# Kernel optimization log

Measured on AMD Instinct MI355X. Metric: run time of the kernel, lower is better.

The kernel has to match this reference:

```python
import jax, jax.numpy as jnp
import numpy as np

D_MODEL = 1024
NUM_HEADS = 16
HEAD_DIM = D_MODEL // NUM_HEADS
BATCH = 4
SEQ = 2048


def circulant(x, c, b):
    # Circulant linear layer via FFT: y = irfft(rfft(x) * rfft(c)) + b
    # x: (..., d), c: (d,), b: (d,)
    d = c.shape[0]
    y = jnp.fft.irfft(jnp.fft.rfft(x, axis=-1) * jnp.fft.rfft(c), n=d, axis=-1)
    return y + b


def setup_inputs() -> dict:
    key = jax.random.key(0)
    ks = jax.random.split(key, 9)
    scale = 1.0 / np.sqrt(D_MODEL)
    inp = {
        "x": jax.random.normal(ks[0], (BATCH, SEQ, D_MODEL), dtype=jnp.float32),
        "wq_c": jax.random.normal(ks[1], (D_MODEL,), dtype=jnp.float32) * scale,
        "wq_b": jnp.zeros((D_MODEL,), dtype=jnp.float32),
        "wk_c": jax.random.normal(ks[2], (D_MODEL,), dtype=jnp.float32) * scale,
        "wk_b": jnp.zeros((D_MODEL,), dtype=jnp.float32),
        "wv_c": jax.random.normal(ks[3], (D_MODEL,), dtype=jnp.float32) * scale,
        "wv_b": jnp.zeros((D_MODEL,), dtype=jnp.float32),
        "wo_c": jax.random.normal(ks[4], (D_MODEL,), dtype=jnp.float32) * scale,
        "wo_b": jnp.zeros((D_MODEL,), dtype=jnp.float32),
    }
    return inp


def reference(x, wq_c, wq_b, wk_c, wk_b, wv_c, wv_b, wo_c, wo_b):
    bs, seq_len, dm = x.shape
    Q = circulant(x, wq_c, wq_b)  # (B, S, D)
    K = circulant(x, wk_c, wk_b)
    V = circulant(x, wv_c, wv_b)
    Q = Q.reshape(bs, seq_len, NUM_HEADS, HEAD_DIM)
    K = K.reshape(bs, seq_len, NUM_HEADS, HEAD_DIM)
    V = V.reshape(bs, seq_len, NUM_HEADS, HEAD_DIM)
    scale = HEAD_DIM ** (-0.5)
    attn_logits = jnp.einsum("bqhd,bkhd->bhqk", Q, K) * scale  # (B, H, S, S)
    attn_weights = jax.nn.softmax(attn_logits, axis=-1)
    out_heads = jnp.einsum("bhqk,bkhd->bqhd", attn_weights, V)
    out_merge = out_heads.reshape(bs, seq_len, dm)
    out = circulant(out_merge, wo_c, wo_b)
    return out
```

## Files before the change

kernel.cpp:

```cpp
#include <hip/hip_runtime.h>
#include <hip/hip_bf16.h>

#define D_MODEL 1024
#define NUM_HEADS 16
#define HEAD_DIM 64
#define BATCH 4
#define SEQ 2048
#define MROWS (BATCH * SEQ)

using f32x4  = __attribute__((ext_vector_type(4))) float;
using bf16x8 = __attribute__((ext_vector_type(8))) short;

__device__ inline unsigned short f2bf(float f) {
    __hip_bfloat16 h = __float2bfloat16(f);
    return *reinterpret_cast<unsigned short*>(&h);
}

__device__ inline void gld_lds16(const unsigned short* g, unsigned short* l) {
    __builtin_amdgcn_global_load_lds(
        (const __attribute__((address_space(1))) unsigned int*)g,
        (__attribute__((address_space(3))) unsigned int*)l, 16, 0, 0);
}

#define QSCALE 0.18033688011112042f

__global__ __launch_bounds__(256) void prep(
    const float* __restrict__ cq, const float* __restrict__ ck,
    const float* __restrict__ cv, const float* __restrict__ co,
    const float* __restrict__ bq, const float* __restrict__ bk,
    const float* __restrict__ bv, const float* __restrict__ bo,
    unsigned short* __restrict__ Wt, float* __restrict__ bias,
    const float* __restrict__ x, unsigned short* __restrict__ xb)
{
    const int bid = blockIdx.x;
    const int t = threadIdx.x;
    if (bid < 4096) {
        const int n = bid;
        const int sel = n >> 10, nl = n & 1023;
        const float* c  = sel == 0 ? cq : sel == 1 ? ck : sel == 2 ? cv : co;
        const float* bb = sel == 0 ? bq : sel == 1 ? bk : sel == 2 ? bv : bo;
        const float sc = (sel == 0) ? QSCALE : 1.0f;
        ushort4 o;
        o.x = f2bf(sc * c[(nl - (4*t + 0)) & 1023]);
        o.y = f2bf(sc * c[(nl - (4*t + 1)) & 1023]);
        o.z = f2bf(sc * c[(nl - (4*t + 2)) & 1023]);
        o.w = f2bf(sc * c[(nl - (4*t + 3)) & 1023]);
        ((ushort4*)(Wt + (size_t)n * 1024))[t] = o;
        if (t == 0) bias[n] = sc * bb[nl];
    } else {
        const size_t i = (size_t)(bid - 4096) * 1024 + t * 4;
        float4 v = *(const float4*)(x + i);
        ushort4 o;
        o.x = f2bf(v.x); o.y = f2bf(v.y); o.z = f2bf(v.z); o.w = f2bf(v.w);
        *(ushort4*)(xb + i) = o;
    }
}

template <int OUT_MODE>
__global__ __launch_bounds__(256, 3) void gemm_circ(
    const unsigned short* __restrict__ A,
    const unsigned short* __restrict__ Bt,
    const float* __restrict__ bias,
    unsigned short* __restrict__ Qb, unsigned short* __restrict__ Kb,
    unsigned short* __restrict__ Vt, float* __restrict__ Cf)
{
    __shared__ unsigned short As[128 * 64];
    __shared__ unsigned short Bs[128 * 64];
    const int t = threadIdx.x;
    const int w = t >> 6, lane = t & 63;
    const int quad = lane >> 4, l16 = lane & 15;
    const int m0 = blockIdx.x * 128;
    const int n0 = blockIdx.y * 128;
    const int wm = (w & 1) * 64, wn = (w >> 1) * 64;

    f32x4 acc[4][4];
#pragma unroll
    for (int i = 0; i < 4; ++i)
#pragma unroll
        for (int j = 0; j < 4; ++j) acc[i][j] = (f32x4){0.f, 0.f, 0.f, 0.f};

    for (int k0 = 0; k0 < 1024; k0 += 64) {
        __syncthreads();
#pragma unroll
        for (int j = 0; j < 4; ++j) {
            const int s = j * 4 + w;
            const int i = s * 64 + lane;
            const int r = i >> 3;
            const int c = (i & 7) ^ (r & 7);
            gld_lds16(A  + (size_t)(m0 + r) * 1024 + k0 + c * 8, &As[s * 512]);
            gld_lds16(Bt + (size_t)(n0 + r) * 1024 + k0 + c * 8, &Bs[s * 512]);
        }
        __syncthreads();

#pragma unroll
        for (int kk = 0; kk < 2; ++kk) {
            bf16x8 af[4], bfr[4];
#pragma unroll
            for (int i = 0; i < 4; ++i) {
                const int r = wm + i * 16 + l16;
                const int slot = r * 8 + ((kk * 4 + quad) ^ (r & 7));
                af[i] = *(const bf16x8*)&As[slot * 8];
            }
#pragma unroll
            for (int j = 0; j < 4; ++j) {
                const int r = wn + j * 16 + l16;
                const int slot = r * 8 + ((kk * 4 + quad) ^ (r & 7));
                bfr[j] = *(const bf16x8*)&Bs[slot * 8];
            }
#pragma unroll
            for (int i = 0; i < 4; ++i)
#pragma unroll
                for (int j = 0; j < 4; ++j)
                    acc[i][j] = __builtin_amdgcn_mfma_f32_16x16x32_bf16(
                        af[i], bfr[j], acc[i][j], 0, 0, 0);
        }
    }

#pragma unroll
    for (int i = 0; i < 4; ++i) {
        const int gm = m0 + wm + i * 16 + quad * 4;
#pragma unroll
        for (int j = 0; j < 4; ++j) {
            const int gn = n0 + wn + j * 16 + l16;
            const float bv = bias[gn];
            if (OUT_MODE == 1) {
#pragma unroll
                for (int rr = 0; rr < 4; ++rr)
                    Cf[(size_t)(gm + rr) * 1024 + gn] = acc[i][j][rr] + bv;
            } else {
                const int sel = gn >> 10;
                if (sel == 0) {
#pragma unroll
                    for (int rr = 0; rr < 4; ++rr)
                        Qb[(size_t)(gm + rr) * 1024 + gn] = f2bf(acc[i][j][rr] + bv);
                } else if (sel == 1) {
                    const int col = gn & 1023;
#pragma unroll
                    for (int rr = 0; rr < 4; ++rr)
                        Kb[(size_t)(gm + rr) * 1024 + col] = f2bf(acc[i][j][rr] + bv);
                } else {
                    const int d = gn & 1023;
                    const int head = d >> 6, dl = d & 63;
                    const int b = gm >> 11, key = gm & 2047;
                    ushort4 vv;
                    vv.x = f2bf(acc[i][j][0] + bv);
                    vv.y = f2bf(acc[i][j][1] + bv);
                    vv.z = f2bf(acc[i][j][2] + bv);
                    vv.w = f2bf(acc[i][j][3] + bv);
                    *(ushort4*)&Vt[((size_t)((b * 16 + head) * 64 + dl)) * 2048 + key] = vv;
                }
            }
        }
    }
}

__global__ __launch_bounds__(256, 4) void attn_mfma(
    const unsigned short* __restrict__ Qb, const unsigned short* __restrict__ Kb,
    const unsigned short* __restrict__ Vt, unsigned short* __restrict__ O)
{
    __shared__ unsigned short Ks[2][64 * 64];
    __shared__ unsigned short Vs[2][64 * 64];

    const int t = threadIdx.x;
    const int w = t >> 6, lane = t & 63;
    const int quad = lane >> 4, l16 = lane & 15;
    const int bh = blockIdx.x;
    const int b = bh >> 4, head = bh & 15;
    const int qbase = blockIdx.y * 128 + w * 32;

    bf16x8 qa[2][2];
#pragma unroll
    for (int s = 0; s < 2; ++s)
#pragma unroll
        for (int h = 0; h < 2; ++h) {
            size_t off = (size_t)(b * SEQ + qbase + s*16 + l16) * D_MODEL
                       + head * HEAD_DIM + h*32 + quad*8;
            qa[s][h] = *(const bf16x8*)(Qb + off);
        }

    f32x4 acc[2][4];
    f32x4 acc_sum[2];
#pragma unroll
    for (int s = 0; s < 2; ++s) {
#pragma unroll
        for (int dt = 0; dt < 4; ++dt) acc[s][dt] = (f32x4){0.f,0.f,0.f,0.f};
        acc_sum[s] = (f32x4){0.f,0.f,0.f,0.f};
    }

    bf16x8 vones;
#pragma unroll
    for (int i = 0; i < 8; ++i) vones[i] = (short)0x3F80;

    const size_t kbase  = (size_t)(b * SEQ) * D_MODEL + head * HEAD_DIM;
    const size_t vtbase = (size_t)((b * NUM_HEADS + head) * HEAD_DIM) * SEQ;

#pragma unroll
    for (int j = 0; j < 2; ++j) {
        const int seg = j * 4 + w;
        const int i = seg * 64 + lane;
        const int r = i >> 3;
        const int ck = (i & 7) ^ ((r & 3) | ((r >> 1) & 4));
        const int cv = (i & 7) ^ (r & 7);
        gld_lds16(Kb + kbase + (size_t)r * D_MODEL + ck * 8, &Ks[0][seg * 512]);
        gld_lds16(Vt + vtbase + (size_t)r * SEQ + cv * 8, &Vs[0][seg * 512]);
    }

    int ib = 0;
    for (int kb = 0; kb < SEQ; kb += 64, ib ^= 1) {
        __syncthreads();

        if (kb + 64 < SEQ) {
#pragma unroll
            for (int j = 0; j < 2; ++j) {
                const int seg = j * 4 + w;
                const int i = seg * 64 + lane;
                const int r = i >> 3;
                const int ck = (i & 7) ^ ((r & 3) | ((r >> 1) & 4));
                const int cv = (i & 7) ^ (r & 7);
                gld_lds16(Kb + kbase + (size_t)(kb + 64 + r) * D_MODEL + ck * 8,
                          &Ks[ib ^ 1][seg * 512]);
                gld_lds16(Vt + vtbase + (size_t)r * SEQ + kb + 64 + cv * 8,
                          &Vs[ib ^ 1][seg * 512]);
            }
        }

        bf16x8 kf[2][2][2];
#pragma unroll
        for (int kh = 0; kh < 2; ++kh)
#pragma unroll
            for (int m = 0; m < 2; ++m) {
                const int r = kh * 32 + ((l16 >> 2) << 3) + m * 4 + (l16 & 3);
                const int sg = (r & 3) | ((r >> 1) & 4);
#pragma unroll
                for (int h = 0; h < 2; ++h) {
                    const int cc = (h * 4 + quad) ^ sg;
                    kf[kh][m][h] = *(const bf16x8*)&Ks[ib][(r * 8 + cc) * 8];
                }
            }

#pragma unroll
        for (int kh = 0; kh < 2; ++kh) {
            bf16x8 pf[2];
#pragma unroll
            for (int s = 0; s < 2; ++s) {
                f32x4 st0 = (f32x4){0.f,0.f,0.f,0.f};
                f32x4 st1 = (f32x4){0.f,0.f,0.f,0.f};
#pragma unroll
                for (int h = 0; h < 2; ++h) {
                    st0 = __builtin_amdgcn_mfma_f32_16x16x32_bf16(
                        kf[kh][0][h], qa[s][h], st0, 0, 0, 0);
                    st1 = __builtin_amdgcn_mfma_f32_16x16x32_bf16(
                        kf[kh][1][h], qa[s][h], st1, 0, 0, 0);
                }
                float p0 = __builtin_amdgcn_exp2f(st0[0]);
                float p1 = __builtin_amdgcn_exp2f(st0[1]);
                float p2 = __builtin_amdgcn_exp2f(st0[2]);
                float p3 = __builtin_amdgcn_exp2f(st0[3]);
                float p4 = __builtin_amdgcn_exp2f(st1[0]);
                float p5 = __builtin_amdgcn_exp2f(st1[1]);
                float p6 = __builtin_amdgcn_exp2f(st1[2]);
                float p7 = __builtin_amdgcn_exp2f(st1[3]);
                __hip_bfloat162 w0 = __float22bfloat162_rn(make_float2(p0, p1));
                __hip_bfloat162 w1 = __float22bfloat162_rn(make_float2(p2, p3));
                __hip_bfloat162 w2 = __float22bfloat162_rn(make_float2(p4, p5));
                __hip_bfloat162 w3 = __float22bfloat162_rn(make_float2(p6, p7));
                union { bf16x8 v; unsigned int u[4]; } pu;
                pu.u[0] = *reinterpret_cast<unsigned int*>(&w0);
                pu.u[1] = *reinterpret_cast<unsigned int*>(&w1);
                pu.u[2] = *reinterpret_cast<unsigned int*>(&w2);
                pu.u[3] = *reinterpret_cast<unsigned int*>(&w3);
                pf[s] = pu.v;
            }

#pragma unroll
            for (int dt = 0; dt < 4; ++dt) {
                const int r = dt * 16 + l16;
                const int cv = (kh * 4 + quad) ^ (r & 7);
                bf16x8 vf = *(const bf16x8*)&Vs[ib][(r * 8 + cv) * 8];
#pragma unroll
                for (int s = 0; s < 2; ++s)
                    acc[s][dt] = __builtin_amdgcn_mfma_f32_16x16x32_bf16(
                        pf[s], vf, acc[s][dt], 0, 0, 0);
            }
#pragma unroll
            for (int s = 0; s < 2; ++s)
                acc_sum[s] = __builtin_amdgcn_mfma_f32_16x16x32_bf16(
                    pf[s], vones, acc_sum[s], 0, 0, 0);
        }
    }

#pragma unroll
    for (int s = 0; s < 2; ++s)
#pragma unroll
        for (int rr = 0; rr < 4; ++rr) {
            float inv = 1.0f / acc_sum[s][rr];
            int q = qbase + s*16 + quad*4 + rr;
            unsigned short* orow = O + (size_t)(b * SEQ + q) * D_MODEL + head * HEAD_DIM + l16;
#pragma unroll
            for (int dt = 0; dt < 4; ++dt) orow[dt*16] = f2bf(acc[s][dt][rr] * inv);
        }
}

extern "C" void kernel_launch(void* const* d_in, const int* in_sizes, int n_in,
                              void* d_out, int out_size, void* d_ws, size_t ws_size,
                              hipStream_t stream) {
    const float* x    = (const float*)d_in[0];
    const float* wq_c = (const float*)d_in[1];
    const float* wq_b = (const float*)d_in[2];
    const float* wk_c = (const float*)d_in[3];
    const float* wk_b = (const float*)d_in[4];
    const float* wv_c = (const float*)d_in[5];
    const float* wv_b = (const float*)d_in[6];
    const float* wo_c = (const float*)d_in[7];
    const float* wo_b = (const float*)d_in[8];
    float* out = (float*)d_out;

    char* ws = (char*)d_ws;
    unsigned short* Wt   = (unsigned short*)(ws);
    float*          bias = (float*)(ws + ((size_t)8  << 20));
    unsigned short* xb   = (unsigned short*)(ws + ((size_t)10 << 20));
    unsigned short* Qb   = (unsigned short*)(ws + ((size_t)26 << 20));
    unsigned short* Kb   = (unsigned short*)(ws + ((size_t)42 << 20));
    unsigned short* Vt   = (unsigned short*)(ws + ((size_t)58 << 20));
    unsigned short* Ob   = (unsigned short*)(ws + ((size_t)74 << 20));

    prep<<<4096 + MROWS, 256, 0, stream>>>(wq_c, wk_c, wv_c, wo_c,
                                           wq_b, wk_b, wv_b, wo_b,
                                           Wt, bias, x, xb);
    gemm_circ<0><<<dim3(64, 24), 256, 0, stream>>>(xb, Wt, bias, Qb, Kb, Vt, nullptr);
    attn_mfma<<<dim3(BATCH * NUM_HEADS, SEQ / 128), 256, 0, stream>>>(Qb, Kb, Vt, Ob);
    gemm_circ<1><<<dim3(64, 8), 256, 0, stream>>>(Ob, Wt + (size_t)3072 * 1024,
                                                  bias + 3072, nullptr, nullptr, nullptr, out);
}
```

Baseline: 246.8 us.

## Use 512-thread attention blocks sharing K/V tiles and remap GEMM blocks across XCDs

The attention kernel now runs 8 waves per block over 256 queries, so each K/V tile loaded into LDS serves twice as many query rows and each thread issues one load per tile instead of two. This halves K/V global traffic per query and the per-thread load count, at the cost of larger blocks and fewer blocks in the grid. The GEMM kernels also remap the flat block index so that consecutive tiles land on the same XCD chiplet, which should improve L2 reuse of the A and B tiles. Launch bounds of 512 threads with 4 blocks may constrain registers.

Result: slower. 278.7 us (+13.0%).

```diff
diff --git a/kernel.cpp b/kernel.cpp
--- a/kernel.cpp
+++ b/kernel.cpp
@@ -69,8 +69,12 @@
     const int t = threadIdx.x;
     const int w = t >> 6, lane = t & 63;
     const int quad = lane >> 4, l16 = lane & 15;
-    const int m0 = blockIdx.x * 128;
-    const int n0 = blockIdx.y * 128;
+
+    const int flat = blockIdx.y * gridDim.x + blockIdx.x;
+    const int cpx  = (gridDim.x * gridDim.y) >> 3;
+    const int nf   = (flat & 7) * cpx + (flat >> 3);
+    const int m0 = (nf % gridDim.x) * 128;
+    const int n0 = (nf / gridDim.x) * 128;
     const int wm = (w & 1) * 64, wn = (w >> 1) * 64;
 
     f32x4 acc[4][4];
@@ -154,7 +158,7 @@
     }
 }
 
-__global__ __launch_bounds__(256, 4) void attn_mfma(
+__global__ __launch_bounds__(512, 4) void attn_mfma(
     const unsigned short* __restrict__ Qb, const unsigned short* __restrict__ Kb,
     const unsigned short* __restrict__ Vt, unsigned short* __restrict__ O)
 {
@@ -166,7 +170,7 @@
     const int quad = lane >> 4, l16 = lane & 15;
     const int bh = blockIdx.x;
     const int b = bh >> 4, head = bh & 15;
-    const int qbase = blockIdx.y * 128 + w * 32;
+    const int qbase = blockIdx.y * 256 + w * 32;
 
     bf16x8 qa[2][2];
 #pragma unroll
@@ -194,34 +198,22 @@
     const size_t kbase  = (size_t)(b * SEQ) * D_MODEL + head * HEAD_DIM;
     const size_t vtbase = (size_t)((b * NUM_HEADS + head) * HEAD_DIM) * SEQ;
 
-#pragma unroll
-    for (int j = 0; j < 2; ++j) {
-        const int seg = j * 4 + w;
-        const int i = seg * 64 + lane;
-        const int r = i >> 3;
-        const int ck = (i & 7) ^ ((r & 3) | ((r >> 1) & 4));
-        const int cv = (i & 7) ^ (r & 7);
-        gld_lds16(Kb + kbase + (size_t)r * D_MODEL + ck * 8, &Ks[0][seg * 512]);
-        gld_lds16(Vt + vtbase + (size_t)r * SEQ + cv * 8, &Vs[0][seg * 512]);
-    }
+    const int r  = t >> 3;
+    const int ck = (t & 7) ^ ((r & 3) | ((r >> 1) & 4));
+    const int cv = (t & 7) ^ (r & 7);
+
+    gld_lds16(Kb + kbase + (size_t)r * D_MODEL + ck * 8, &Ks[0][w * 512]);
+    gld_lds16(Vt + vtbase + (size_t)r * SEQ + cv * 8, &Vs[0][w * 512]);
 
     int ib = 0;
     for (int kb = 0; kb < SEQ; kb += 64, ib ^= 1) {
         __syncthreads();
 
         if (kb + 64 < SEQ) {
-#pragma unroll
-            for (int j = 0; j < 2; ++j) {
-                const int seg = j * 4 + w;
-                const int i = seg * 64 + lane;
-                const int r = i >> 3;
-                const int ck = (i & 7) ^ ((r & 3) | ((r >> 1) & 4));
-                const int cv = (i & 7) ^ (r & 7);
-                gld_lds16(Kb + kbase + (size_t)(kb + 64 + r) * D_MODEL + ck * 8,
-                          &Ks[ib ^ 1][seg * 512]);
-                gld_lds16(Vt + vtbase + (size_t)r * SEQ + kb + 64 + cv * 8,
-                          &Vs[ib ^ 1][seg * 512]);
-            }
+            gld_lds16(Kb + kbase + (size_t)(kb + 64 + r) * D_MODEL + ck * 8,
+                      &Ks[ib ^ 1][w * 512]);
+            gld_lds16(Vt + vtbase + (size_t)r * SEQ + kb + 64 + cv * 8,
+                      &Vs[ib ^ 1][w * 512]);
         }
 
         bf16x8 kf[2][2][2];
@@ -229,12 +221,12 @@
         for (int kh = 0; kh < 2; ++kh)
 #pragma unroll
             for (int m = 0; m < 2; ++m) {
-                const int r = kh * 32 + ((l16 >> 2) << 3) + m * 4 + (l16 & 3);
-                const int sg = (r & 3) | ((r >> 1) & 4);
+                const int rk = kh * 32 + ((l16 >> 2) << 3) + m * 4 + (l16 & 3);
+                const int sg = (rk & 3) | ((rk >> 1) & 4);
 #pragma unroll
                 for (int h = 0; h < 2; ++h) {
                     const int cc = (h * 4 + quad) ^ sg;
-                    kf[kh][m][h] = *(const bf16x8*)&Ks[ib][(r * 8 + cc) * 8];
+                    kf[kh][m][h] = *(const bf16x8*)&Ks[ib][(rk * 8 + cc) * 8];
                 }
             }
 
@@ -274,9 +266,9 @@
 
 #pragma unroll
             for (int dt = 0; dt < 4; ++dt) {
-                const int r = dt * 16 + l16;
-                const int cv = (kh * 4 + quad) ^ (r & 7);
-                bf16x8 vf = *(const bf16x8*)&Vs[ib][(r * 8 + cv) * 8];
+                const int rv = dt * 16 + l16;
+                const int cvv = (kh * 4 + quad) ^ (rv & 7);
+                bf16x8 vf = *(const bf16x8*)&Vs[ib][(rv * 8 + cvv) * 8];
 #pragma unroll
                 for (int s = 0; s < 2; ++s)
                     acc[s][dt] = __builtin_amdgcn_mfma_f32_16x16x32_bf16(
@@ -328,7 +320,7 @@
                                            wq_b, wk_b, wv_b, wo_b,
                                            Wt, bias, x, xb);
     gemm_circ<0><<<dim3(64, 24), 256, 0, stream>>>(xb, Wt, bias, Qb, Kb, Vt, nullptr);
-    attn_mfma<<<dim3(BATCH * NUM_HEADS, SEQ / 128), 256, 0, stream>>>(Qb, Kb, Vt, Ob);
+    attn_mfma<<<dim3(BATCH * NUM_HEADS, SEQ / 256), 512, 0, stream>>>(Qb, Kb, Vt, Ob);
     gemm_circ<1><<<dim3(64, 8), 256, 0, stream>>>(Ob, Wt + (size_t)3072 * 1024,
                                                   bias + 3072, nullptr, nullptr, nullptr, out);
 }
```
